# Kernel optimization log

Measured on AMD Instinct MI355X. Metric: run time of the kernel, lower is better.

The kernel has to match this reference:

```python
import jax, jax.numpy as jnp
import numpy as np

B, S, NB = 2, 1024, 64
V, D, L, H, F = 1024, 512, 12, 8, 2048
DH = D // H
MAX_BARS = 256


def _ln(x, g, b):
    m = x.mean(-1, keepdims=True)
    v = ((x - m) ** 2).mean(-1, keepdims=True)
    return (x - m) * jax.lax.rsqrt(v + 1e-5) * g + b


def _rope(x, pos):
    # x: (B, T, H, DH), pos: (T,)
    half = x.shape[-1] // 2
    inv = 10000.0 ** (-jnp.arange(half, dtype=jnp.float32) / half)
    f = pos.astype(jnp.float32)[:, None] * inv  # (T, half)
    cos = jnp.cos(f)[None, :, None, :]
    sin = jnp.sin(f)[None, :, None, :]
    x1, x2 = x[..., :half], x[..., half:]
    return jnp.concatenate([x1 * cos - x2 * sin, x1 * sin + x2 * cos], -1)


def _swiglu(h, w1, w3, w2):
    return (jax.nn.silu(h @ w1) * (h @ w3)) @ w2


def _attention(sum_x, x, Wq, Wk, Wv, Wo, smask, umask, pos_s, pos_r):
    # shared QKV/O projections over both streams; 4-way block mask via concat keys
    b, nb, _ = sum_x.shape
    s = x.shape[1]

    def proj(t, W):
        return (t @ W).reshape(t.shape[0], t.shape[1], H, DH)

    qs = _rope(proj(sum_x, Wq), pos_s)
    qr = _rope(proj(x, Wq), pos_r)
    k = jnp.concatenate([_rope(proj(sum_x, Wk), pos_s), _rope(proj(x, Wk), pos_r)], 1)
    v = jnp.concatenate([proj(sum_x, Wv), proj(x, Wv)], 1)
    scale = DH ** -0.5

    def attend(q, mask):
        sc = jnp.einsum('bqhd,bkhd->bhqk', q, k) * scale
        sc = jnp.where(mask[:, None], sc, -1e9)
        p = jax.nn.softmax(sc, axis=-1)
        o = jnp.einsum('bhqk,bkhd->bqhd', p, v)
        return o.reshape(q.shape[0], q.shape[1], D)

    return attend(qs, smask) @ Wo, attend(qr, umask) @ Wo


def _forward(tok_emb, inst_emb, bar_emb,
             ln_as_g, ln_as_b, ln_ar_g, ln_ar_b,
             ln_fs_g, ln_fs_b, ln_fr_g, ln_fr_b,
             Wq, Wk, Wv, Wo,
             fs_w1, fs_w3, fs_w2, fr_w1, fr_w3, fr_w2,
             out_g, out_b,
             token_ids, chord_ids, instrument_ids, num_bars):
    b, s = token_ids.shape
    nb = num_bars
    x = tok_emb[token_ids] + inst_emb[jnp.clip(instrument_ids, 0, 129)]
    sum_x = jnp.broadcast_to(bar_emb[:nb][None], (b, nb, tok_emb.shape[1]))

    bars = jnp.arange(nb)
    idx = jnp.arange(s)
    # ss: summary b attends summaries b' <= b (causal over bars)
    ss = jnp.broadcast_to(jnp.tril(jnp.ones((nb, nb), bool))[None], (b, nb, nb))
    # sr: summary b summarizes regular tokens in bar b
    sr = chord_ids[:, None, :] == bars[None, :, None]  # (B, nb, S)
    smask = jnp.concatenate([ss, sr], -1)  # (B, nb, nb+S)
    # rs: regular i attends summaries of strictly previous bars
    rs = bars[None, None, :] < chord_ids[:, :, None]  # (B, S, nb)
    # rr: regular i attends regular j in same bar, causally
    rr = (chord_ids[:, :, None] == chord_ids[:, None, :]) & (idx[:, None] >= idx[None, :])
    umask = jnp.concatenate([rs, rr], -1)  # (B, S, nb+S)

    pos_s = jnp.arange(nb)
    pos_r = jnp.arange(s)

    for l in range(Wq.shape[0]):
        a_s, a_r = _attention(_ln(sum_x, ln_as_g[l], ln_as_b[l]),
                              _ln(x, ln_ar_g[l], ln_ar_b[l]),
                              Wq[l], Wk[l], Wv[l], Wo[l], smask, umask, pos_s, pos_r)
        sum_x = sum_x + a_s
        x = x + a_r
        sum_x = sum_x + _swiglu(_ln(sum_x, ln_fs_g[l], ln_fs_b[l]), fs_w1[l], fs_w3[l], fs_w2[l])
        x = x + _swiglu(_ln(x, ln_fr_g[l], ln_fr_b[l]), fr_w1[l], fr_w3[l], fr_w2[l])

    x = _ln(x, out_g, out_b)
    return x @ tok_emb.T  # tied lm_head


def setup_inputs():
    key = jax.random.key(0)
    it = iter(jax.random.split(key, 40))

    def nrm(shape):
        return jax.random.normal(next(it), shape, jnp.float32) * 0.02

    inp = {
        'token_ids': jax.random.randint(next(it), (B, S), 0, V),
        'chord_ids': jnp.sort(jax.random.randint(next(it), (B, S), 0, NB), axis=-1),
        'instrument_ids': jax.random.randint(next(it), (B, S), 0, 130),
        'num_bars': NB,
        'tok_emb': nrm((V, D)),
        'inst_emb': nrm((130, D)),
        'bar_emb': nrm((MAX_BARS, D)),
        'ln_as_g': jnp.ones((L, D)), 'ln_as_b': jnp.zeros((L, D)),
        'ln_ar_g': jnp.ones((L, D)), 'ln_ar_b': jnp.zeros((L, D)),
        'ln_fs_g': jnp.ones((L, D)), 'ln_fs_b': jnp.zeros((L, D)),
        'ln_fr_g': jnp.ones((L, D)), 'ln_fr_b': jnp.zeros((L, D)),
        'Wq': nrm((L, D, D)), 'Wk': nrm((L, D, D)),
        'Wv': nrm((L, D, D)), 'Wo': nrm((L, D, D)),
        'fs_w1': nrm((L, D, F)), 'fs_w3': nrm((L, D, F)), 'fs_w2': nrm((L, F, D)),
        'fr_w1': nrm((L, D, F)), 'fr_w3': nrm((L, D, F)), 'fr_w2': nrm((L, F, D)),
        'out_g': jnp.ones((D,)), 'out_b': jnp.zeros((D,)),
    }
    return inp


def reference(token_ids, chord_ids, instrument_ids, num_bars,
              tok_emb, inst_emb, bar_emb,
              ln_as_g, ln_as_b, ln_ar_g, ln_ar_b,
              ln_fs_g, ln_fs_b, ln_fr_g, ln_fr_b,
              Wq, Wk, Wv, Wo,
              fs_w1, fs_w3, fs_w2, fr_w1, fr_w3, fr_w2,
              out_g, out_b):
    return _forward(tok_emb, inst_emb, bar_emb,
                    ln_as_g, ln_as_b, ln_ar_g, ln_ar_b,
                    ln_fs_g, ln_fs_b, ln_fr_g, ln_fr_b,
                    Wq, Wk, Wv, Wo,
                    fs_w1, fs_w3, fs_w2, fr_w1, fr_w3, fr_w2,
                    out_g, out_b,
                    token_ids, chord_ids, instrument_ids, num_bars)
```

## Files before the change

kernel.cpp:

```cpp
#include <hip/hip_runtime.h>
#include <stdint.h>

#define NB 64
#define BATCH 2
#define SEQ 1024
#define DMODEL 512
#define NHEAD 8
#define DHEAD 64
#define FDIM 2048
#define NLAYER 12
#define VOCAB 1024
#define KTOT (NB + SEQ)
#define RSUM (BATCH * NB)
#define RREG (BATCH * SEQ)
#define RTOT (RSUM + RREG)

using bf16x8 = __attribute__((ext_vector_type(8))) short;
using bf16x4 = __attribute__((ext_vector_type(4))) short;
using f32x4  = __attribute__((ext_vector_type(4))) float;

__device__ __forceinline__ unsigned short f2bf(float f) {
  union { float f; unsigned u; } c; c.f = f;
  return (unsigned short)((c.u + 0x7fffu + ((c.u >> 16) & 1u)) >> 16);
}
__device__ __forceinline__ float bf2f(unsigned short s) {
  union { unsigned u; float f; } c; c.u = ((unsigned)s) << 16;
  return c.f;
}

template<int R>
__device__ __forceinline__ void stage_tile(
    const unsigned short* __restrict__ G, int K, int base_row, int k0,
    unsigned short (*lds)[64], int wid, int lane)
{
  const int rl = lane >> 3;
  const int j  = lane & 7;
  #pragma unroll
  for (int c = 0; c < R / 32; ++c) {
    const int r0 = wid * (R / 4) + c * 8;
    const int row = r0 + rl;
    const unsigned short* g = G + (size_t)(base_row + row) * K + k0
                                + ((j ^ (row & 7)) << 3);
    __builtin_amdgcn_global_load_lds(
        (const __attribute__((address_space(1))) void*)g,
        (__attribute__((address_space(3))) void*)&lds[r0][0], 16, 0, 0);
  }
}

template<int R>
__device__ __forceinline__ void stage_tile_blk(
    const unsigned short* __restrict__ G, int ntiles, int tile_n, int bnoff,
    int k0, unsigned short (*lds)[64], int wid, int lane)
{
  const unsigned short* __restrict__ T =
      G + ((size_t)(k0 >> 6) * ntiles + tile_n) * 4096;
  const int rl = lane >> 3;
  const int j  = lane & 7;
  #pragma unroll
  for (int c = 0; c < R / 32; ++c) {
    const int r0 = wid * (R / 4) + c * 8;
    const int row = r0 + rl;
    const unsigned short* g = T + (size_t)(bnoff + row) * 64
                                + ((j ^ (row & 7)) << 3);
    __builtin_amdgcn_global_load_lds(
        (const __attribute__((address_space(1))) void*)g,
        (__attribute__((address_space(3))) void*)&lds[r0][0], 16, 0, 0);
  }
}

__device__ __forceinline__ bf16x8 lds_frag(const unsigned short (*lds)[64],
                                           int row, int cc) {
  return *(const bf16x8*)&lds[row][(cc ^ (row & 7)) << 3];
}

template<int BM, int BN, int EPI, bool PIPE, bool BBLK>
__global__ __launch_bounds__(256) void gemm_bt(
    const unsigned short* __restrict__ A, const unsigned short* __restrict__ B0,
    const unsigned short* __restrict__ B1,
    void* __restrict__ Cout, const float* resid, int N, int K, int nbt,
    const float* __restrict__ cost, const float* __restrict__ sint,
    unsigned short* __restrict__ kcat, unsigned short* __restrict__ vcat)
{
  constexpr int BK = 64;
  constexpr int WM = BM / 2, WN = BN / 2;
  constexpr int FM = WM / 16, FN = WN / 16;
  constexpr int HALF = (BM + BN) * BK * 2;
  constexpr int SM_STAGE = (PIPE ? 2 : 1) * HALF;
  constexpr int SM_CT = (EPI == 3) ? 64 * 66 * 4 : 0;
  constexpr int SMSZ = SM_STAGE > SM_CT ? SM_STAGE : SM_CT;
  __shared__ __align__(16) unsigned char smem[SMSZ];
  const int bm = blockIdx.y * BM, bn = blockIdx.x * BN;
  const unsigned short* __restrict__ BT = (bm < RSUM) ? B0 : B1;
  const int tn = bn >> 6, bnoff = bn & 63;
  const int tid = threadIdx.x;
  const int wid = tid >> 6, lane = tid & 63;
  const int wm = wid >> 1, wn = wid & 1;
  const int lr = lane & 15, lk = lane >> 4;
  f32x4 acc[FM][FN] = {};
  auto stageB = [&](int k0, unsigned short (*lds)[64]) {
    if constexpr (BBLK) stage_tile_blk<BN>(BT, nbt, tn, bnoff, k0, lds, wid, lane);
    else stage_tile<BN>(BT, K, bn, k0, lds, wid, lane);
  };
  if constexpr (PIPE) {
    auto AsB = [&](int b) { return (unsigned short (*)[BK])(smem + b * HALF); };
    auto BsB = [&](int b) { return (unsigned short (*)[BK])(smem + b * HALF + BM * BK * 2); };
    stage_tile<BM>(A, K, bm, 0, AsB(0), wid, lane);
    stageB(0, BsB(0));
    __syncthreads();
    int cur = 0;
    for (int k0 = 0; k0 < K; k0 += BK) {
      if (k0 + BK < K) {
        stage_tile<BM>(A, K, bm, k0 + BK, AsB(cur ^ 1), wid, lane);
        stageB(k0 + BK, BsB(cur ^ 1));
      }
      #pragma unroll
      for (int kk = 0; kk < 2; ++kk) {
        bf16x8 af[FM], bfr[FN];
        #pragma unroll
        for (int m = 0; m < FM; ++m)
          af[m] = lds_frag(AsB(cur), wm * WM + m * 16 + lr, kk * 4 + lk);
        #pragma unroll
        for (int n = 0; n < FN; ++n)
          bfr[n] = lds_frag(BsB(cur), wn * WN + n * 16 + lr, kk * 4 + lk);
        #pragma unroll
        for (int m = 0; m < FM; ++m)
          #pragma unroll
          for (int n = 0; n < FN; ++n)
            acc[m][n] = __builtin_amdgcn_mfma_f32_16x16x32_bf16(af[m], bfr[n], acc[m][n], 0, 0, 0);
      }
      __syncthreads();
      cur ^= 1;
    }
  } else {
    auto As = (unsigned short (*)[BK])smem;
    auto Bs = (unsigned short (*)[BK])(smem + BM * BK * 2);
    for (int k0 = 0; k0 < K; k0 += BK) {
      __syncthreads();
      stage_tile<BM>(A, K, bm, k0, As, wid, lane);
      stageB(k0, Bs);
      __syncthreads();
      #pragma unroll
      for (int kk = 0; kk < 2; ++kk) {
        bf16x8 af[FM], bfr[FN];
        #pragma unroll
        for (int m = 0; m < FM; ++m)
          af[m] = lds_frag(As, wm * WM + m * 16 + lr, kk * 4 + lk);
        #pragma unroll
        for (int n = 0; n < FN; ++n)
          bfr[n] = lds_frag(Bs, wn * WN + n * 16 + lr, kk * 4 + lk);
        #pragma unroll
        for (int m = 0; m < FM; ++m)
          #pragma unroll
          for (int n = 0; n < FN; ++n)
            acc[m][n] = __builtin_amdgcn_mfma_f32_16x16x32_bf16(af[m], bfr[n], acc[m][n], 0, 0, 0);
      }
    }
  }
  if constexpr (EPI == 3) {
    __syncthreads();
    auto ct = (float (*)[66])smem;
    #pragma unroll
    for (int m = 0; m < FM; ++m)
      #pragma unroll
      for (int n = 0; n < FN; ++n)
        #pragma unroll
        for (int i = 0; i < 4; ++i)
          ct[wm * WM + m * 16 + lk * 4 + i][wn * WN + n * 16 + lr] = acc[m][n][i];
    __syncthreads();
    const int r = tid >> 2, quad = tid & 3;
    const int tr = bm + r;
    int b, pos, catrow;
    if (tr < RSUM) { b = tr >> 6; pos = tr & (NB - 1); catrow = pos; }
    else { const int rr = tr - RSUM; b = rr >> 10; pos = rr & (SEQ - 1); catrow = NB + pos; }
    const int part = bn >> 9;
    const int head = (bn & 511) >> 6;
    const size_t obase = ((size_t)(b * NHEAD + head) * KTOT + catrow) * DHEAD + quad * 16;
    union { unsigned short u[16]; uint4 q[2]; } ob;
    if (part == 2) {
      #pragma unroll
      for (int j = 0; j < 16; ++j) ob.u[j] = f2bf(ct[r][quad * 16 + j]);
      *(uint4*)&vcat[obase] = ob.q[0];
      *(uint4*)&vcat[obase + 8] = ob.q[1];
    } else {
      #pragma unroll
      for (int j = 0; j < 16; ++j) {
        const int d = quad * 16 + j;
        const float v = ct[r][d];
        const float other = ct[r][d ^ 32];
        const float cs = cost[pos * 32 + (d & 31)];
        const float sn = sint[pos * 32 + (d & 31)];
        ob.u[j] = f2bf((d < 32) ? (v * cs - other * sn) : (other * sn + v * cs));
      }
      unsigned short* dst = part ? kcat : (unsigned short*)Cout;
      *(uint4*)&dst[obase] = ob.q[0];
      *(uint4*)&dst[obase + 8] = ob.q[1];
    }
    return;
  }
  #pragma unroll
  for (int m = 0; m < FM; ++m)
    #pragma unroll
    for (int n = 0; n < FN; ++n)
      #pragma unroll
      for (int i = 0; i < 4; ++i) {
        int row = bm + wm * WM + m * 16 + lk * 4 + i;
        int col = bn + wn * WN + n * 16 + lr;
        float v = acc[m][n][i];
        if constexpr (EPI == 1) {
          const float other = __shfl_xor(v, 1, 64);
          if (!(lr & 1)) {
            const float g = v, u = other;
            const float hv = (g / (1.f + __expf(-g))) * u;
            unsigned short* C = (unsigned short*)Cout;
            C[(size_t)row * (N >> 1) + (col >> 1)] = f2bf(hv);
          }
        } else if constexpr (EPI == 2) {
          unsigned short* C = (unsigned short*)Cout;
          C[(size_t)row * N + col] = f2bf(v);
        } else {
          float* C = (float*)Cout;
          size_t idx = (size_t)row * N + col;
          if (resid) v += resid[idx];
          C[idx] = v;
        }
      }
}

template<bool ILV>
__global__ __launch_bounds__(256) void transpose_blk_kernel(
    const float* __restrict__ a0, const float* __restrict__ b0,
    const float* __restrict__ a1, const float* __restrict__ b1,
    const float* __restrict__ a2, const float* __restrict__ b2,
    const float* __restrict__ a3, const float* __restrict__ b3,
    unsigned short* d0_, unsigned short* d1_,
    unsigned short* d2_, unsigned short* d3_,
    int Nsrc, size_t sstride, size_t dstride,
    int4 ntiles, int4 otbase, int nlayer)
{
  __shared__ float tile[64][65];
  const int fam = blockIdx.z / nlayer, l = blockIdx.z % nlayer;
  const float* sa = (fam == 0 ? a0 : fam == 1 ? a1 : fam == 2 ? a2 : a3)
                    + (size_t)l * sstride;
  const float* sb = ILV ? ((fam == 0 ? b0 : fam == 1 ? b1 : fam == 2 ? b2 : b3)
                    + (size_t)l * sstride) : nullptr;
  unsigned short* d = (fam == 0 ? d0_ : fam == 1 ? d1_ : fam == 2 ? d2_ : d3_)
                    + (size_t)l * dstride;
  const int nt  = fam == 0 ? ntiles.x : fam == 1 ? ntiles.y : fam == 2 ? ntiles.z : ntiles.w;
  const int otb = fam == 0 ? otbase.x : fam == 1 ? otbase.y : fam == 2 ? otbase.z : otbase.w;
  const int kt = blockIdx.y, ot = blockIdx.x;
  const int k0 = kt * 64;
  const int rr = threadIdx.x >> 4, c4 = threadIdx.x & 15;
  #pragma unroll
  for (int it = 0; it < 4; ++it) {
    const int r = rr + it * 16;
    const float* s;
    int col0;
    if constexpr (ILV) {
      s = (c4 < 8) ? sa : sb;
      col0 = ot * 32 + (c4 & 7) * 4;
    } else {
      s = sa;
      col0 = ot * 64 + c4 * 4;
    }
    *(float4*)&tile[r][c4 * 4] = *(const float4*)&s[(size_t)(k0 + r) * Nsrc + col0];
  }
  __syncthreads();
  const int r = threadIdx.x >> 2, j = threadIdx.x & 3;
  const int col = ILV ? ((r >> 1) | ((r & 1) << 5)) : r;
  union { unsigned short u[16]; uint4 q[2]; } ob;
  #pragma unroll
  for (int i = 0; i < 16; ++i) ob.u[i] = f2bf(tile[j * 16 + i][col]);
  unsigned short* drow = d + ((size_t)kt * nt + otb + ot) * 4096 + r * 64 + j * 16;
  *(uint4*)&drow[0] = ob.q[0];
  *(uint4*)&drow[8] = ob.q[1];
}

__global__ __launch_bounds__(256) void convert_bf16_kernel(
    const float* __restrict__ src, unsigned short* __restrict__ dst)
{
  const int i = (blockIdx.x * 256 + threadIdx.x) * 4;
  const float4 v = *(const float4*)&src[i];
  union { unsigned short u[4]; uint2 q; } o;
  o.u[0] = f2bf(v.x); o.u[1] = f2bf(v.y); o.u[2] = f2bf(v.z); o.u[3] = f2bf(v.w);
  *(uint2*)&dst[i] = o.q;
}

__global__ __launch_bounds__(128) void embed_kernel(
    const int* __restrict__ tok, const int* __restrict__ inst,
    const float* __restrict__ tok_emb, const float* __restrict__ inst_emb,
    const float* __restrict__ bar_emb, float* __restrict__ z)
{
  const int r = blockIdx.x, t = threadIdx.x;
  float4 val;
  if (r < RSUM) {
    const int bar = r & (NB - 1);
    val = *(const float4*)&bar_emb[(size_t)bar * DMODEL + t * 4];
  } else {
    const int rr = r - RSUM;
    const int b = rr >> 10, i = rr & (SEQ - 1);
    const int tk = tok[b * SEQ + i];
    int ins = inst[b * SEQ + i];
    ins = ins < 0 ? 0 : (ins > 129 ? 129 : ins);
    const float4 a = *(const float4*)&tok_emb[(size_t)tk * DMODEL + t * 4];
    const float4 cc = *(const float4*)&inst_emb[(size_t)ins * DMODEL + t * 4];
    val.x = a.x + cc.x; val.y = a.y + cc.y; val.z = a.z + cc.z; val.w = a.w + cc.w;
  }
  *(float4*)&z[(size_t)r * DMODEL + t * 4] = val;
}

__global__ __launch_bounds__(256) void ln_dual_kernel(
    const float* __restrict__ x, const float* __restrict__ g_s,
    const float* __restrict__ b_s, const float* __restrict__ g_r,
    const float* __restrict__ b_r, unsigned short* __restrict__ out)
{
  const int wid = threadIdx.x >> 6, lane = threadIdx.x & 63;
  const size_t row = (size_t)blockIdx.x * 4 + wid;
  const float* g = (row < RSUM) ? g_s : g_r;
  const float* bb = (row < RSUM) ? b_s : b_r;
  const float* xr = x + row * DMODEL + lane * 8;
  float v[8];
  *(float4*)&v[0] = *(const float4*)&xr[0];
  *(float4*)&v[4] = *(const float4*)&xr[4];
  float s = 0.f;
  #pragma unroll
  for (int j = 0; j < 8; ++j) s += v[j];
  #pragma unroll
  for (int o = 32; o > 0; o >>= 1) s += __shfl_xor(s, o, 64);
  const float mean = s * (1.f / DMODEL);
  float vs = 0.f;
  #pragma unroll
  for (int j = 0; j < 8; ++j) { float d = v[j] - mean; vs += d * d; }
  #pragma unroll
  for (int o = 32; o > 0; o >>= 1) vs += __shfl_xor(vs, o, 64);
  const float rs = rsqrtf(vs * (1.f / DMODEL) + 1e-5f);
  float gg[8], bv[8];
  *(float4*)&gg[0] = *(const float4*)&g[lane * 8];
  *(float4*)&gg[4] = *(const float4*)&g[lane * 8 + 4];
  *(float4*)&bv[0] = *(const float4*)&bb[lane * 8];
  *(float4*)&bv[4] = *(const float4*)&bb[lane * 8 + 4];
  union { unsigned short u[8]; uint4 q; } o8;
  #pragma unroll
  for (int j = 0; j < 8; ++j) o8.u[j] = f2bf((v[j] - mean) * rs * gg[j] + bv[j]);
  *(uint4*)&out[row * DMODEL + lane * 8] = o8.q;
}

__global__ __launch_bounds__(256) void ln_kernel(
    const float* __restrict__ x, const float* __restrict__ g,
    const float* __restrict__ bb, unsigned short* __restrict__ out)
{
  const int wid = threadIdx.x >> 6, lane = threadIdx.x & 63;
  const size_t row = (size_t)blockIdx.x * 4 + wid;
  const float* xr = x + row * DMODEL + lane * 8;
  float v[8];
  *(float4*)&v[0] = *(const float4*)&xr[0];
  *(float4*)&v[4] = *(const float4*)&xr[4];
  float s = 0.f;
  #pragma unroll
  for (int j = 0; j < 8; ++j) s += v[j];
  #pragma unroll
  for (int o = 32; o > 0; o >>= 1) s += __shfl_xor(s, o, 64);
  const float mean = s * (1.f / DMODEL);
  float vs = 0.f;
  #pragma unroll
  for (int j = 0; j < 8; ++j) { float d = v[j] - mean; vs += d * d; }
  #pragma unroll
  for (int o = 32; o > 0; o >>= 1) vs += __shfl_xor(vs, o, 64);
  const float rs = rsqrtf(vs * (1.f / DMODEL) + 1e-5f);
  float gg[8], bv[8];
  *(float4*)&gg[0] = *(const float4*)&g[lane * 8];
  *(float4*)&gg[4] = *(const float4*)&g[lane * 8 + 4];
  *(float4*)&bv[0] = *(const float4*)&bb[lane * 8];
  *(float4*)&bv[4] = *(const float4*)&bb[lane * 8 + 4];
  union { unsigned short u[8]; uint4 q; } o8;
  #pragma unroll
  for (int j = 0; j < 8; ++j) o8.u[j] = f2bf((v[j] - mean) * rs * gg[j] + bv[j]);
  *(uint4*)&out[row * DMODEL + lane * 8] = o8.q;
}

__global__ void rope_table_kernel(float* __restrict__ cost, float* __restrict__ sint) {
  const int pos = blockIdx.x, j = threadIdx.x;
  const float inv = powf(10000.f, -(float)j / 32.f);
  const float f = (float)pos * inv;
  cost[pos * 32 + j] = cosf(f);
  sint[pos * 32 + j] = sinf(f);
}

__global__ void segstart_kernel(const int* __restrict__ chord, int* __restrict__ seg) {
  const int b = blockIdx.x, t = threadIdx.x;
  if (t <= NB) {
    int lo = 0, hi = SEQ;
    while (lo < hi) {
      int mid = (lo + hi) >> 1;
      if (chord[b * SEQ + mid] < t) lo = mid + 1; else hi = mid;
    }
    seg[b * (NB + 1) + t] = lo;
  }
}

__global__ __launch_bounds__(256) void attn_kernel(
    const unsigned short* __restrict__ q_cat, const unsigned short* __restrict__ k_cat,
    const unsigned short* __restrict__ v_cat, const int* __restrict__ seg,
    const int* __restrict__ chord, unsigned short* __restrict__ att)
{
  const int h = blockIdx.y, b = blockIdx.z;
  const int wid = threadIdx.x >> 6, lane = threadIdx.x & 63;
  const int qi = blockIdx.x * 4 + wid;
  int qrow, nsum, s0, nk, outrow;
  if (qi < NB) {
    const int c = qi;
    s0 = seg[b * (NB + 1) + c];
    const int s1 = seg[b * (NB + 1) + c + 1];
    qrow = c; nsum = c + 1; nk = nsum + (s1 - s0);
    outrow = b * NB + c;
  } else {
    const int i = qi - NB;
    const int c = chord[b * SEQ + i];
    s0 = seg[b * (NB + 1) + c];
    qrow = NB + i; nsum = c; nk = nsum + (i - s0 + 1);
    outrow = RSUM + b * SEQ + i;
  }
  const size_t bh = (size_t)(b * NHEAD + h) * KTOT * DHEAD;
  const unsigned short* __restrict__ Kp = k_cat + bh;
  const unsigned short* __restrict__ Vp = v_cat + bh;
  __shared__ __align__(16) float qsh[4][DHEAD];
  __shared__ __align__(16) float psh[4][64];
  qsh[wid][lane] = bf2f(q_cat[bh + (size_t)qrow * DHEAD + lane]) * 0.125f;
  const int lq = lane & 3;
  const int lkey = lane >> 2;
  const int kk = lane >> 4;
  const int dd = lane & 15;
  float m = -1e30f, l = 0.f;
  float4 o4 = {0.f, 0.f, 0.f, 0.f};
  for (int t0 = 0; t0 < nk; t0 += 64) {
    float sv[4];
    float tmax = -3.0e38f;
    #pragma unroll
    for (int pass = 0; pass < 4; ++pass) {
      const int t = t0 + pass * 16 + lkey;
      int kr = (t < nsum) ? t : (NB + s0 + (t - nsum));
      if (kr > KTOT - 1) kr = KTOT - 1;
      const bf16x8* krp = (const bf16x8*)(Kp + (size_t)kr * DHEAD + lq * 16);
      const bf16x8 k0v = krp[0], k1v = krp[1];
      float a = 0.f;
      #pragma unroll
      for (int d2 = 0; d2 < 8; ++d2)
        a = fmaf(qsh[wid][lq * 16 + d2], bf2f((unsigned short)k0v[d2]), a);
      #pragma unroll
      for (int d2 = 0; d2 < 8; ++d2)
        a = fmaf(qsh[wid][lq * 16 + 8 + d2], bf2f((unsigned short)k1v[d2]), a);
      a += __shfl_xor(a, 1, 64);
      a += __shfl_xor(a, 2, 64);
      sv[pass] = (t < nk) ? a : -3.0e38f;
      tmax = fmaxf(tmax, sv[pass]);
    }
    #pragma unroll
    for (int off = 32; off > 0; off >>= 1) tmax = fmaxf(tmax, __shfl_xor(tmax, off, 64));
    const float mn = fmaxf(m, tmax);
    float psum = 0.f;
    #pragma unroll
    for (int pass = 0; pass < 4; ++pass) {
      const float pp = __expf(sv[pass] - mn);
      psum += pp;
      if (lq == 0) psh[wid][pass * 16 + lkey] = pp;
    }
    psum *= 0.25f;
    #pragma unroll
    for (int off = 32; off > 0; off >>= 1) psum += __shfl_xor(psum, off, 64);
    const float scale = __expf(m - mn);
    l = l * scale + psum;
    o4.x *= scale; o4.y *= scale; o4.z *= scale; o4.w *= scale;
    m = mn;
    #pragma unroll
    for (int j = 0; j < 16; ++j) {
      const int toff = j * 4 + kk;
      const float p = psh[wid][toff];
      const int tk = t0 + toff;
      int kr = (tk < nsum) ? tk : (NB + s0 + (tk - nsum));
      if (kr > KTOT - 1) kr = KTOT - 1;
      const bf16x4 vv = *(const bf16x4*)&Vp[(size_t)kr * DHEAD + dd * 4];
      o4.x = fmaf(p, bf2f((unsigned short)vv[0]), o4.x);
      o4.y = fmaf(p, bf2f((unsigned short)vv[1]), o4.y);
      o4.z = fmaf(p, bf2f((unsigned short)vv[2]), o4.z);
      o4.w = fmaf(p, bf2f((unsigned short)vv[3]), o4.w);
    }
  }
  #pragma unroll
  for (int off = 16; off <= 32; off <<= 1) {
    o4.x += __shfl_xor(o4.x, off, 64);
    o4.y += __shfl_xor(o4.y, off, 64);
    o4.z += __shfl_xor(o4.z, off, 64);
    o4.w += __shfl_xor(o4.w, off, 64);
  }
  if (kk == 0) {
    const float invl = 1.f / l;
    union { unsigned short u[4]; uint2 q; } ob;
    ob.u[0] = f2bf(o4.x * invl); ob.u[1] = f2bf(o4.y * invl);
    ob.u[2] = f2bf(o4.z * invl); ob.u[3] = f2bf(o4.w * invl);
    *(uint2*)&att[(size_t)outrow * DMODEL + h * DHEAD + dd * 4] = ob.q;
  }
}

extern "C" void kernel_launch(void* const* d_in, const int* in_sizes, int n_in,
                              void* d_out, int out_size, void* d_ws, size_t ws_size,
                              hipStream_t stream)
{
  const int* tok      = (const int*)d_in[0];
  const int* chord    = (const int*)d_in[1];
  const int* inst     = (const int*)d_in[2];
  const float* tok_emb  = (const float*)d_in[4];
  const float* inst_emb = (const float*)d_in[5];
  const float* bar_emb  = (const float*)d_in[6];
  const float* ln_as_g = (const float*)d_in[7];
  const float* ln_as_b = (const float*)d_in[8];
  const float* ln_ar_g = (const float*)d_in[9];
  const float* ln_ar_b = (const float*)d_in[10];
  const float* ln_fs_g = (const float*)d_in[11];
  const float* ln_fs_b = (const float*)d_in[12];
  const float* ln_fr_g = (const float*)d_in[13];
  const float* ln_fr_b = (const float*)d_in[14];
  const float* Wq = (const float*)d_in[15];
  const float* Wk = (const float*)d_in[16];
  const float* Wv = (const float*)d_in[17];
  const float* Wo = (const float*)d_in[18];
  const float* fs_w1 = (const float*)d_in[19];
  const float* fs_w3 = (const float*)d_in[20];
  const float* fs_w2 = (const float*)d_in[21];
  const float* fr_w1 = (const float*)d_in[22];
  const float* fr_w3 = (const float*)d_in[23];
  const float* fr_w2 = (const float*)d_in[24];
  const float* out_g = (const float*)d_in[25];
  const float* out_b = (const float*)d_in[26];

  char* p = (char*)d_ws;
  auto alloc = [&](size_t bytes) -> void* {
    void* r = (void*)p;
    p += (bytes + 255) & ~(size_t)255;
    return r;
  };
  unsigned short* WqkvT  = (unsigned short*)alloc((size_t)NLAYER * 1536 * 512 * 2);
  unsigned short* WoT    = (unsigned short*)alloc((size_t)NLAYER * 512 * 512 * 2);
  unsigned short* fsW13T = (unsigned short*)alloc((size_t)NLAYER * 4096 * 512 * 2);
  unsigned short* frW13T = (unsigned short*)alloc((size_t)NLAYER * 4096 * 512 * 2);
  unsigned short* fsW2T  = (unsigned short*)alloc((size_t)NLAYER * 512 * 2048 * 2);
  unsigned short* frW2T  = (unsigned short*)alloc((size_t)NLAYER * 512 * 2048 * 2);
  unsigned short* tokT   = (unsigned short*)alloc((size_t)VOCAB * DMODEL * 2);
  float* z           = (float*)alloc((size_t)RTOT * DMODEL * 4);
  unsigned short* zn = (unsigned short*)alloc((size_t)RTOT * DMODEL * 2);
  unsigned short* q_cat = (unsigned short*)alloc((size_t)BATCH * NHEAD * KTOT * DHEAD * 2);
  unsigned short* k_cat = (unsigned short*)alloc((size_t)BATCH * NHEAD * KTOT * DHEAD * 2);
  unsigned short* v_cat = (unsigned short*)alloc((size_t)BATCH * NHEAD * KTOT * DHEAD * 2);
  unsigned short* att = (unsigned short*)alloc((size_t)RTOT * DMODEL * 2);
  unsigned short* h1 = (unsigned short*)alloc((size_t)RTOT * FDIM * 2);
  float* cost        = (float*)alloc((size_t)SEQ * 32 * 4);
  float* sint        = (float*)alloc((size_t)SEQ * 32 * 4);
  int* seg           = (int*)alloc((size_t)BATCH * (NB + 1) * 4);
  if ((size_t)(p - (char*)d_ws) > ws_size) return;

  transpose_blk_kernel<false><<<dim3(8, 8, 3 * NLAYER), 256, 0, stream>>>(
      Wq, nullptr, Wk, nullptr, Wv, nullptr, nullptr, nullptr,
      WqkvT, WqkvT, WqkvT, WqkvT,
      512, (size_t)512 * 512, (size_t)1536 * 512,
      make_int4(24, 24, 24, 24), make_int4(0, 8, 16, 0), NLAYER);
  transpose_blk_kernel<false><<<dim3(8, 8, NLAYER), 256, 0, stream>>>(
      Wo, nullptr, nullptr, nullptr, nullptr, nullptr, nullptr, nullptr,
      WoT, WoT, WoT, WoT,
      512, (size_t)512 * 512, (size_t)512 * 512,
      make_int4(8, 8, 8, 8), make_int4(0, 0, 0, 0), NLAYER);
  transpose_blk_kernel<true><<<dim3(64, 8, 2 * NLAYER), 256, 0, stream>>>(
      fs_w1, fs_w3, fr_w1, fr_w3, nullptr, nullptr, nullptr, nullptr,
      fsW13T, frW13T, fsW13T, frW13T,
      2048, (size_t)512 * 2048, (size_t)4096 * 512,
      make_int4(64, 64, 64, 64), make_int4(0, 0, 0, 0), NLAYER);
  transpose_blk_kernel<false><<<dim3(8, 32, 2 * NLAYER), 256, 0, stream>>>(
      fs_w2, nullptr, fr_w2, nullptr, nullptr, nullptr, nullptr, nullptr,
      fsW2T, frW2T, fsW2T, frW2T,
      512, (size_t)2048 * 512, (size_t)512 * 2048,
      make_int4(8, 8, 8, 8), make_int4(0, 0, 0, 0), NLAYER);
  convert_bf16_kernel<<<VOCAB * DMODEL / 1024, 256, 0, stream>>>(tok_emb, tokT);

  embed_kernel<<<RTOT, 128, 0, stream>>>(tok, inst, tok_emb, inst_emb, bar_emb, z);
  rope_table_kernel<<<SEQ, 32, 0, stream>>>(cost, sint);
  segstart_kernel<<<BATCH, 128, 0, stream>>>(chord, seg);

  for (int l = 0; l < NLAYER; ++l) {
    const size_t ld = (size_t)l * DMODEL;
    ln_dual_kernel<<<RTOT / 4, 256, 0, stream>>>(z, ln_as_g + ld, ln_as_b + ld,
                                                 ln_ar_g + ld, ln_ar_b + ld, zn);
    gemm_bt<64, 64, 3, false, true><<<dim3(1536 / 64, RTOT / 64), 256, 0, stream>>>(
        zn, WqkvT + (size_t)l * 1536 * 512, WqkvT + (size_t)l * 1536 * 512,
        q_cat, nullptr, 1536, 512, 24, cost, sint, k_cat, v_cat);
    attn_kernel<<<dim3(KTOT / 4, NHEAD, BATCH), 256, 0, stream>>>(q_cat, k_cat, v_cat, seg, chord, att);
    gemm_bt<32, 32, 0, true, true><<<dim3(512 / 32, RTOT / 32), 256, 0, stream>>>(
        att, WoT + (size_t)l * 512 * 512, WoT + (size_t)l * 512 * 512,
        z, z, 512, 512, 8, nullptr, nullptr, nullptr, nullptr);
    ln_dual_kernel<<<RTOT / 4, 256, 0, stream>>>(z, ln_fs_g + ld, ln_fs_b + ld,
                                                 ln_fr_g + ld, ln_fr_b + ld, zn);
    gemm_bt<64, 64, 1, false, true><<<dim3(4096 / 64, RTOT / 64), 256, 0, stream>>>(
        zn, fsW13T + (size_t)l * 4096 * 512, frW13T + (size_t)l * 4096 * 512,
        h1, nullptr, 4096, 512, 64, nullptr, nullptr, nullptr, nullptr);
    gemm_bt<32, 32, 0, true, true><<<dim3(512 / 32, RTOT / 32), 256, 0, stream>>>(
        h1, fsW2T + (size_t)l * 512 * 2048, frW2T + (size_t)l * 512 * 2048,
        z, z, 512, 2048, 8, nullptr, nullptr, nullptr, nullptr);
  }

  ln_kernel<<<RREG / 4, 256, 0, stream>>>(z + (size_t)RSUM * DMODEL, out_g, out_b,
                                          zn + (size_t)RSUM * DMODEL);
  gemm_bt<32, 32, 0, true, false><<<dim3(VOCAB / 32, RREG / 32), 256, 0, stream>>>(
      zn + (size_t)RSUM * DMODEL, tokT, tokT, (float*)d_out, nullptr, VOCAB, 512,
      0, nullptr, nullptr, nullptr, nullptr);
}
```

Before: 1.224 ms.

## Store W1/W3 unpacked and gather gate/up columns in SwiGLU GEMM staging

The weight-conversion kernel is rewritten to convert each 64x512 fp32 block to bf16 in shared memory first and then write 64-wide blocked transposed tiles. W1 and W3 are now stored as separate halves instead of column-interleaved. The SwiGLU GEMM's B staging gathers matching W1 and W3 rows so each warp's two N-fragments hold the gate and up values for the same columns. This lets the epilogue combine them in registers without a cross-lane shuffle and without half the lanes sitting idle. The trade-off is a hardcoded staging path that assumes a specific BN and warp layout, plus a larger shared-memory tile in the transpose kernel.

```diff
diff --git a/kernel.cpp b/kernel.cpp
--- a/kernel.cpp
+++ b/kernel.cpp
@@ -98,8 +98,31 @@
   const int lr = lane & 15, lk = lane >> 4;
   f32x4 acc[FM][FN] = {};
   auto stageB = [&](int k0, unsigned short (*lds)[64]) {
-    if constexpr (BBLK) stage_tile_blk<BN>(BT, nbt, tn, bnoff, k0, lds, wid, lane);
-    else stage_tile<BN>(BT, K, bn, k0, lds, wid, lane);
+    if constexpr (EPI == 1) {
+      const int f0 = bn >> 1;
+      const unsigned short* w3p = BT + (size_t)2048 * 512;
+      const int tf = f0 >> 6, rb = f0 & 63;
+      const int rl = lane >> 3, j = lane & 7;
+      #pragma unroll
+      for (int c = 0; c < 2; ++c) {
+        const int g = wid * 2 + c;
+        const int s_ = g >> 1, h = g & 1;
+        const unsigned short* base = (s_ & 1) ? w3p : BT;
+        const int srcrow = rb + (s_ >> 1) * 16 + h * 8 + rl;
+        const int lr0 = g * 8;
+        const int ldsrow = lr0 + rl;
+        const unsigned short* gp = base + ((size_t)(k0 >> 6) * 32 + tf) * 4096
+                                     + (size_t)srcrow * 64
+                                     + ((j ^ (ldsrow & 7)) << 3);
+        __builtin_amdgcn_global_load_lds(
+            (const __attribute__((address_space(1))) void*)gp,
+            (__attribute__((address_space(3))) void*)&lds[lr0][0], 16, 0, 0);
+      }
+    } else if constexpr (BBLK) {
+      stage_tile_blk<BN>(BT, nbt, tn, bnoff, k0, lds, wid, lane);
+    } else {
+      stage_tile<BN>(BT, K, bn, k0, lds, wid, lane);
+    }
   };
   if constexpr (PIPE) {
     auto AsB = [&](int b) { return (unsigned short (*)[BK])(smem + b * HALF); };
@@ -197,6 +220,21 @@
     }
     return;
   }
+  if constexpr (EPI == 1) {
+    unsigned short* C = (unsigned short*)Cout;
+    #pragma unroll
+    for (int m = 0; m < FM; ++m)
+      #pragma unroll
+      for (int i = 0; i < 4; ++i) {
+        const int row = bm + wm * WM + m * 16 + lk * 4 + i;
+        const int col = (bn >> 1) + wn * 16 + lr;
+        const float g = acc[m][0][i];
+        const float u = acc[m][1][i];
+        const float hv = (g / (1.f + __expf(-g))) * u;
+        C[(size_t)row * (N >> 1) + col] = f2bf(hv);
+      }
+    return;
+  }
   #pragma unroll
   for (int m = 0; m < FM; ++m)
     #pragma unroll
@@ -206,15 +244,7 @@
         int row = bm + wm * WM + m * 16 + lk * 4 + i;
         int col = bn + wn * WN + n * 16 + lr;
         float v = acc[m][n][i];
-        if constexpr (EPI == 1) {
-          const float other = __shfl_xor(v, 1, 64);
-          if (!(lr & 1)) {
-            const float g = v, u = other;
-            const float hv = (g / (1.f + __expf(-g))) * u;
-            unsigned short* C = (unsigned short*)Cout;
-            C[(size_t)row * (N >> 1) + (col >> 1)] = f2bf(hv);
-          }
-        } else if constexpr (EPI == 2) {
+        if constexpr (EPI == 2) {
           unsigned short* C = (unsigned short*)Cout;
           C[(size_t)row * N + col] = f2bf(v);
         } else {
@@ -226,53 +256,57 @@
       }
 }
 
-template<bool ILV>
-__global__ __launch_bounds__(256) void transpose_blk_kernel(
-    const float* __restrict__ a0, const float* __restrict__ b0,
-    const float* __restrict__ a1, const float* __restrict__ b1,
-    const float* __restrict__ a2, const float* __restrict__ b2,
-    const float* __restrict__ a3, const float* __restrict__ b3,
+__global__ __launch_bounds__(256) void transpose_blk2_kernel(
+    const float* __restrict__ a0, const float* __restrict__ a1,
+    const float* __restrict__ a2, const float* __restrict__ a3,
     unsigned short* d0_, unsigned short* d1_,
     unsigned short* d2_, unsigned short* d3_,
-    int Nsrc, size_t sstride, size_t dstride,
-    int4 ntiles, int4 otbase, int nlayer)
-{
-  __shared__ float tile[64][65];
+    int Nsrc, size_t sstride, size_t dstride, int nt, int4 otbase, int nlayer)
+{
+  __shared__ __align__(8) unsigned short tile[64][516];
   const int fam = blockIdx.z / nlayer, l = blockIdx.z % nlayer;
-  const float* sa = (fam == 0 ? a0 : fam == 1 ? a1 : fam == 2 ? a2 : a3)
-                    + (size_t)l * sstride;
-  const float* sb = ILV ? ((fam == 0 ? b0 : fam == 1 ? b1 : fam == 2 ? b2 : b3)
-                    + (size_t)l * sstride) : nullptr;
+  const float* s = (fam == 0 ? a0 : fam == 1 ? a1 : fam == 2 ? a2 : a3)
+                   + (size_t)l * sstride;
   unsigned short* d = (fam == 0 ? d0_ : fam == 1 ? d1_ : fam == 2 ? d2_ : d3_)
-                    + (size_t)l * dstride;
-  const int nt  = fam == 0 ? ntiles.x : fam == 1 ? ntiles.y : fam == 2 ? ntiles.z : ntiles.w;
+                   + (size_t)l * dstride;
   const int otb = fam == 0 ? otbase.x : fam == 1 ? otbase.y : fam == 2 ? otbase.z : otbase.w;
-  const int kt = blockIdx.y, ot = blockIdx.x;
-  const int k0 = kt * 64;
-  const int rr = threadIdx.x >> 4, c4 = threadIdx.x & 15;
-  #pragma unroll
-  for (int it = 0; it < 4; ++it) {
-    const int r = rr + it * 16;
-    const float* s;
-    int col0;
-    if constexpr (ILV) {
-      s = (c4 < 8) ? sa : sb;
-      col0 = ot * 32 + (c4 & 7) * 4;
-    } else {
-      s = sa;
-      col0 = ot * 64 + c4 * 4;
-    }
-    *(float4*)&tile[r][c4 * 4] = *(const float4*)&s[(size_t)(k0 + r) * Nsrc + col0];
+  const int n0 = blockIdx.x * 512, kt = blockIdx.y, k0 = kt * 64;
+  const int wid = threadIdx.x >> 6, lane = threadIdx.x & 63;
+  #pragma unroll 4
+  for (int r = 0; r < 16; ++r) {
+    const int row = wid * 16 + r;
+    #pragma unroll
+    for (int h = 0; h < 2; ++h) {
+      const int col = h * 256 + lane * 4;
+      const float4 v = *(const float4*)&s[(size_t)(k0 + row) * Nsrc + n0 + col];
+      union { unsigned short u[4]; uint2 q; } ob;
+      ob.u[0] = f2bf(v.x); ob.u[1] = f2bf(v.y);
+      ob.u[2] = f2bf(v.z); ob.u[3] = f2bf(v.w);
+      *(uint2*)&tile[row][col] = ob.q;
+    }
   }
   __syncthreads();
-  const int r = threadIdx.x >> 2, j = threadIdx.x & 3;
-  const int col = ILV ? ((r >> 1) | ((r & 1) << 5)) : r;
-  union { unsigned short u[16]; uint4 q[2]; } ob;
-  #pragma unroll
-  for (int i = 0; i < 16; ++i) ob.u[i] = f2bf(tile[j * 16 + i][col]);
-  unsigned short* drow = d + ((size_t)kt * nt + otb + ot) * 4096 + r * 64 + j * 16;
-  *(uint4*)&drow[0] = ob.q[0];
-  *(uint4*)&drow[8] = ob.q[1];
+  const int t = threadIdx.x;
+  const int ot = t >> 5;
+  const int nloc = (2 * t) & 63;
+  unsigned short* tb = d + ((size_t)kt * nt + otb + blockIdx.x * 8 + ot) * 4096;
+  #pragma unroll
+  for (int kc = 0; kc < 4; ++kc) {
+    unsigned v[16];
+    #pragma unroll
+    for (int j2 = 0; j2 < 16; ++j2)
+      v[j2] = *(const unsigned*)&tile[kc * 16 + j2][2 * t - ot * 64 + ot * 64];
+    unsigned lo[8], hi[8];
+    #pragma unroll
+    for (int q2 = 0; q2 < 8; ++q2) {
+      lo[q2] = (v[2 * q2] & 0xffffu) | (v[2 * q2 + 1] << 16);
+      hi[q2] = (v[2 * q2] >> 16) | (v[2 * q2 + 1] & 0xffff0000u);
+    }
+    *(uint4*)&tb[(size_t)nloc * 64 + kc * 16]           = *(uint4*)&lo[0];
+    *(uint4*)&tb[(size_t)nloc * 64 + kc * 16 + 8]       = *(uint4*)&lo[4];
+    *(uint4*)&tb[(size_t)(nloc + 1) * 64 + kc * 16]     = *(uint4*)&hi[0];
+    *(uint4*)&tb[(size_t)(nloc + 1) * 64 + kc * 16 + 8] = *(uint4*)&hi[4];
+  }
 }
 
 __global__ __launch_bounds__(256) void convert_bf16_kernel(
@@ -556,26 +590,22 @@
   int* seg           = (int*)alloc((size_t)BATCH * (NB + 1) * 4);
   if ((size_t)(p - (char*)d_ws) > ws_size) return;
 
-  transpose_blk_kernel<false><<<dim3(8, 8, 3 * NLAYER), 256, 0, stream>>>(
-      Wq, nullptr, Wk, nullptr, Wv, nullptr, nullptr, nullptr,
-      WqkvT, WqkvT, WqkvT, WqkvT,
-      512, (size_t)512 * 512, (size_t)1536 * 512,
-      make_int4(24, 24, 24, 24), make_int4(0, 8, 16, 0), NLAYER);
-  transpose_blk_kernel<false><<<dim3(8, 8, NLAYER), 256, 0, stream>>>(
-      Wo, nullptr, nullptr, nullptr, nullptr, nullptr, nullptr, nullptr,
-      WoT, WoT, WoT, WoT,
-      512, (size_t)512 * 512, (size_t)512 * 512,
-      make_int4(8, 8, 8, 8), make_int4(0, 0, 0, 0), NLAYER);
-  transpose_blk_kernel<true><<<dim3(64, 8, 2 * NLAYER), 256, 0, stream>>>(
-      fs_w1, fs_w3, fr_w1, fr_w3, nullptr, nullptr, nullptr, nullptr,
-      fsW13T, frW13T, fsW13T, frW13T,
-      2048, (size_t)512 * 2048, (size_t)4096 * 512,
-      make_int4(64, 64, 64, 64), make_int4(0, 0, 0, 0), NLAYER);
-  transpose_blk_kernel<false><<<dim3(8, 32, 2 * NLAYER), 256, 0, stream>>>(
-      fs_w2, nullptr, fr_w2, nullptr, nullptr, nullptr, nullptr, nullptr,
-      fsW2T, frW2T, fsW2T, frW2T,
-      512, (size_t)2048 * 512, (size_t)512 * 2048,
-      make_int4(8, 8, 8, 8), make_int4(0, 0, 0, 0), NLAYER);
+  transpose_blk2_kernel<<<dim3(1, 8, 3 * NLAYER), 256, 0, stream>>>(
+      Wq, Wk, Wv, nullptr,
+      WqkvT, WqkvT, WqkvT, nullptr,
+      512, (size_t)512 * 512, (size_t)1536 * 512, 24, make_int4(0, 8, 16, 0), NLAYER);
+  transpose_blk2_kernel<<<dim3(1, 8, NLAYER), 256, 0, stream>>>(
+      Wo, nullptr, nullptr, nullptr,
+      WoT, nullptr, nullptr, nullptr,
+      512, (size_t)512 * 512, (size_t)512 * 512, 8, make_int4(0, 0, 0, 0), NLAYER);
+  transpose_blk2_kernel<<<dim3(4, 8, 4 * NLAYER), 256, 0, stream>>>(
+      fs_w1, fs_w3, fr_w1, fr_w3,
+      fsW13T, fsW13T + (size_t)2048 * 512, frW13T, frW13T + (size_t)2048 * 512,
+      2048, (size_t)512 * 2048, (size_t)4096 * 512, 32, make_int4(0, 0, 0, 0), NLAYER);
+  transpose_blk2_kernel<<<dim3(1, 32, 2 * NLAYER), 256, 0, stream>>>(
+      fs_w2, fr_w2, nullptr, nullptr,
+      fsW2T, frW2T, nullptr, nullptr,
+      512, (size_t)2048 * 512, (size_t)512 * 2048, 8, make_int4(0, 0, 0, 0), NLAYER);
   convert_bf16_kernel<<<VOCAB * DMODEL / 1024, 256, 0, stream>>>(tok_emb, tokT);
 
   embed_kernel<<<RTOT, 128, 0, stream>>>(tok, inst, tok_emb, inst_emb, bar_emb, z);
```

New measurement: 1.237 ms. About the same (+1.0%).
